# Optimization experiments

Hardware: AMD Instinct MI355X
Metric: run time of the kernel (lower is better)

Reference implementation:

```python
import jax, jax.numpy as jnp
import numpy as np

ALPHA = 0.25
GAMMA = 2.0
# all cost weights are 1.0 per init defaults

def box_cxcywh_to_xyxy(b):
    cx, cy, w, h = b[..., 0], b[..., 1], b[..., 2], b[..., 3]
    return jnp.stack([cx - 0.5 * w, cy - 0.5 * h, cx + 0.5 * w, cy + 0.5 * h], axis=-1)

def generalized_box_iou(b1, b2):
    # b1: [B,Q,4], b2: [B,T,4] in xyxy -> [B,Q,T]
    area1 = (b1[..., 2] - b1[..., 0]) * (b1[..., 3] - b1[..., 1])  # [B,Q]
    area2 = (b2[..., 2] - b2[..., 0]) * (b2[..., 3] - b2[..., 1])  # [B,T]
    lt = jnp.maximum(b1[:, :, None, :2], b2[:, None, :, :2])        # [B,Q,T,2]
    rb = jnp.minimum(b1[:, :, None, 2:], b2[:, None, :, 2:])
    wh = jnp.clip(rb - lt, 0.0)
    inter = wh[..., 0] * wh[..., 1]
    union = area1[:, :, None] + area2[:, None, :] - inter
    iou = inter / union
    lt_c = jnp.minimum(b1[:, :, None, :2], b2[:, None, :, :2])
    rb_c = jnp.maximum(b1[:, :, None, 2:], b2[:, None, :, 2:])
    wh_c = jnp.clip(rb_c - lt_c, 0.0)
    area_c = wh_c[..., 0] * wh_c[..., 1]
    return iou - (area_c - union) / area_c

def point_sample_bilinear(img, pts):
    # img: [B,N,H,W]; pts: [P,2] (x,y) in [0,1]. Matches F.grid_sample
    # bilinear, align_corners=False, padding_mode='zeros'.
    H, W = img.shape[-2], img.shape[-1]
    x = pts[:, 0] * W - 0.5
    y = pts[:, 1] * H - 0.5
    x0 = jnp.floor(x); y0 = jnp.floor(y)
    wx1 = x - x0; wx0 = 1.0 - wx1
    wy1 = y - y0; wy0 = 1.0 - wy1

    def gather(yi, xi):
        valid = ((xi >= 0) & (xi < W) & (yi >= 0) & (yi < H)).astype(img.dtype)
        xc = jnp.clip(xi, 0, W - 1).astype(jnp.int32)
        yc = jnp.clip(yi, 0, H - 1).astype(jnp.int32)
        return img[:, :, yc, xc] * valid  # [B,N,P]

    return (gather(y0, x0) * (wy0 * wx0)
            + gather(y0, x0 + 1) * (wy0 * wx1)
            + gather(y0 + 1, x0) * (wy1 * wx0)
            + gather(y0 + 1, x0 + 1) * (wy1 * wx1))

def point_sample_nearest(img, pts):
    # grid_sample nearest, align_corners=False, zeros padding
    H, W = img.shape[-2], img.shape[-1]
    x = jnp.round(pts[:, 0] * W - 0.5)
    y = jnp.round(pts[:, 1] * H - 0.5)
    valid = ((x >= 0) & (x < W) & (y >= 0) & (y < H)).astype(img.dtype)
    xc = jnp.clip(x, 0, W - 1).astype(jnp.int32)
    yc = jnp.clip(y, 0, H - 1).astype(jnp.int32)
    return img[:, :, yc, xc] * valid  # [B,N,P]

def setup_inputs() -> dict:
    key = jax.random.key(0)
    ks = jax.random.split(key, 7)
    B, Q, C, T, H, W = 2, 900, 91, 64, 128, 128
    P = H * W // 16  # mask_point_sample_ratio = 16
    return {
        "pred_logits": jax.random.normal(ks[0], (B, Q, C), jnp.float32),
        "pred_boxes": jax.random.uniform(ks[1], (B, Q, 4), jnp.float32),
        "pred_masks": jax.random.normal(ks[2], (B, Q, H, W), jnp.float32),
        "tgt_boxes": jax.random.uniform(ks[3], (B, T, 4), jnp.float32),
        "tgt_masks": jax.random.uniform(ks[4], (B, T, H, W), jnp.float32),
        "point_coords": jax.random.uniform(ks[5], (1, P, 2), jnp.float32),
        "tgt_labels": jax.random.randint(ks[6], (B, T), 0, C, jnp.int32),
    }

def reference(pred_logits, pred_boxes, pred_masks, tgt_boxes, tgt_masks, point_coords, tgt_labels):
    # ---- focal classification cost ----
    prob = jax.nn.sigmoid(pred_logits)                          # [B,Q,C]
    neg_cost = (1 - ALPHA) * prob ** GAMMA * (-jax.nn.log_sigmoid(-pred_logits))
    pos_cost = ALPHA * (1 - prob) ** GAMMA * (-jax.nn.log_sigmoid(pred_logits))
    diff = pos_cost - neg_cost                                   # [B,Q,C]
    cost_class = jnp.take_along_axis(diff, tgt_labels[:, None, :], axis=2)  # [B,Q,T]

    # ---- L1 bbox cost (cdist p=1) ----
    cost_bbox = jnp.abs(pred_boxes[:, :, None, :] - tgt_boxes[:, None, :, :]).sum(-1)

    # ---- GIoU cost ----
    giou = generalized_box_iou(box_cxcywh_to_xyxy(pred_boxes), box_cxcywh_to_xyxy(tgt_boxes))

    # ---- point-sampled mask CE / Dice costs ----
    pts = point_coords[0]                                        # [P,2]
    P = pts.shape[0]
    pred_pts = point_sample_bilinear(pred_masks, pts)            # [B,Q,P]
    tgt_pts = point_sample_nearest(tgt_masks, pts)               # [B,T,P]
    pos_ce = -jax.nn.log_sigmoid(pred_pts)
    neg_ce = -jax.nn.log_sigmoid(-pred_pts)
    cost_ce = (jnp.einsum('bqp,btp->bqt', pos_ce, tgt_pts)
               + jnp.einsum('bqp,btp->bqt', neg_ce, 1.0 - tgt_pts)) / P
    s = jax.nn.sigmoid(pred_pts)
    numer = 2.0 * jnp.einsum('bqp,btp->bqt', s, tgt_pts)
    denom = s.sum(-1)[:, :, None] + tgt_pts.sum(-1)[:, None, :]
    cost_dice = 1.0 - (numer + 1.0) / (denom + 1.0)

    C = (cost_bbox + cost_class - giou + cost_ce + cost_dice).astype(jnp.float32)
    # replace non-finite entries by 2 * (per-batch max finite cost)
    fin = jnp.isfinite(C)
    max_cost = jnp.max(jnp.where(fin, C, 0.0), axis=(1, 2), keepdims=True)
    C = jnp.where(fin, C, 2.0 * max_cost)
    return C
```

## Files before the change

### kernel.cpp

```cpp
#include <hip/hip_runtime.h>
#include <hip/hip_bf16.h>
#include <math.h>

#define B_    2
#define Q_    900
#define QPAD_ 912
#define MT_   57
#define CC_   91
#define T_    64
#define H_    128
#define W_    128
#define HW_   (H_*W_)
#define P_    1024
#define NIMG_ (B_*T_ + B_*Q_)
#define IPB_  8
#define FLT_BIG 3.402823466e+38f

#define AS1 __attribute__((address_space(1)))
#define AS3 __attribute__((address_space(3)))

typedef short short8 __attribute__((ext_vector_type(8)));
typedef float f32x4  __attribute__((ext_vector_type(4)));

static __device__ __forceinline__ unsigned short f2bf(float v) {
    __hip_bfloat16 h = __float2bfloat16(v);
    return *reinterpret_cast<unsigned short*>(&h);
}

__global__ __launch_bounds__(256) void kS_sample(
    const float* __restrict__ tgt_masks,
    const float* __restrict__ pred_masks,
    const float* __restrict__ pc,
    unsigned short* __restrict__ tgtPT,
    float* __restrict__ tsumP,
    unsigned short* __restrict__ xsbuf,
    float* __restrict__ lnegP,
    float* __restrict__ lsumP,
    float* __restrict__ bmax)
{
    __shared__ float bufA[HW_];
    __shared__ float bufB[HW_];

    const int tid = threadIdx.x;
    const int wv = tid >> 6, lane = tid & 63;
    const int img0 = blockIdx.x * IPB_;
    const bool isTgt = (img0 < B_*T_);

    if (blockIdx.x == 0 && tid < B_) bmax[tid] = 0.f;

    int   nidx[4];
    int   o[4][4]; float ww[4][4];
    if (isTgt) {
        #pragma unroll
        for (int k = 0; k < 4; ++k) {
            int p = tid*4 + k;
            float px = pc[2*p], py = pc[2*p+1];
            float xf = rintf(px * (float)W_ - 0.5f);
            float yf = rintf(py * (float)H_ - 0.5f);
            bool nv = (xf >= 0.f) && (xf < (float)W_) && (yf >= 0.f) && (yf < (float)H_);
            int xc = (int)fminf(fmaxf(xf, 0.f), (float)(W_-1));
            int yc = (int)fminf(fmaxf(yf, 0.f), (float)(H_-1));
            nidx[k] = nv ? (yc*W_ + xc) : -1;
        }
    } else {
        #pragma unroll
        for (int k = 0; k < 4; ++k) {
            int p = tid*4 + k;
            float px = pc[2*p], py = pc[2*p+1];
            float x = px * (float)W_ - 0.5f;
            float y = py * (float)H_ - 0.5f;
            float x0f = floorf(x), y0f = floorf(y);
            float wx1 = x - x0f, wy1 = y - y0f;
            float wx0 = 1.f - wx1, wy0 = 1.f - wy1;
            int x0 = (int)x0f, y0 = (int)y0f;
            int   xs2[2] = {x0, x0+1}, ys2[2] = {y0, y0+1};
            float wxs[2] = {wx0, wx1}, wys[2] = {wy0, wy1};
            #pragma unroll
            for (int dy = 0; dy < 2; ++dy)
            #pragma unroll
            for (int dx = 0; dx < 2; ++dx) {
                int xi = xs2[dx], yi = ys2[dy];
                bool v = (xi >= 0) && (xi < W_) && (yi >= 0) && (yi < H_);
                int xcc = min(max(xi, 0), W_-1);
                int ycc = min(max(yi, 0), H_-1);
                o [k][dy*2+dx] = ycc*W_ + xcc;
                ww[k][dy*2+dx] = v ? wys[dy]*wxs[dx] : 0.f;
            }
        }
    }

    auto STAGE = [&](int im, float* buf) {
        const float* g = ((im < B_*T_) ? (tgt_masks  + (size_t)im * HW_)
                                       : (pred_masks + (size_t)(im - B_*T_) * HW_))
                         + wv*4096 + lane*4;
        float* l = buf + wv*4096;
        #pragma unroll
        for (int it = 0; it < 16; ++it)
            __builtin_amdgcn_global_load_lds((const AS1 float*)(g + it*256),
                                             (AS3 float*)(l + it*256), 16, 0, 0);
    };

    auto SAMPLE = [&](int im, const float* S) {
        if (isTgt) {
            float vals[4];
            #pragma unroll
            for (int k = 0; k < 4; ++k)
                vals[k] = (nidx[k] >= 0) ? S[nidx[k]] : 0.f;
            *(ushort4*)(tgtPT + (size_t)im*P_ + tid*4) =
                make_ushort4(f2bf(vals[0]), f2bf(vals[1]), f2bf(vals[2]), f2bf(vals[3]));
            float local = (vals[0] + vals[1]) + (vals[2] + vals[3]);
            #pragma unroll
            for (int off = 32; off; off >>= 1) local += __shfl_down(local, off);
            if (lane == 0) tsumP[im*4 + wv] = local;
        } else {
            const int bq = im - B_*T_;
            const int b = bq / Q_, q = bq % Q_;
            float tap[4][4];
            #pragma unroll
            for (int k = 0; k < 4; ++k) {
                tap[k][0] = S[o[k][0]]; tap[k][1] = S[o[k][1]];
                tap[k][2] = S[o[k][2]]; tap[k][3] = S[o[k][3]];
            }
            float ln = 0.f, ls = 0.f;
            unsigned short px_[4], ps_[4];
            #pragma unroll
            for (int k = 0; k < 4; ++k) {
                float x = ww[k][0]*tap[k][0] + ww[k][1]*tap[k][1]
                        + ww[k][2]*tap[k][2] + ww[k][3]*tap[k][3];
                float e  = __expf(-fabsf(x));
                float sp = __logf(1.f + e) + fmaxf(x, 0.f);
                float rr = 1.f / (1.f + e);
                float s  = (x >= 0.f) ? rr : e * rr;
                ln += sp; ls += s;
                px_[k] = f2bf(x); ps_[k] = f2bf(s);
            }
            *(ushort4*)(xsbuf + ((size_t)(b*2+0)*QPAD_ + q)*P_ + tid*4) = make_ushort4(px_[0],px_[1],px_[2],px_[3]);
            *(ushort4*)(xsbuf + ((size_t)(b*2+1)*QPAD_ + q)*P_ + tid*4) = make_ushort4(ps_[0],ps_[1],ps_[2],ps_[3]);
            #pragma unroll
            for (int off = 32; off; off >>= 1) {
                ln += __shfl_down(ln, off);
                ls += __shfl_down(ls, off);
            }
            if (lane == 0) {
                lnegP[(b*Q_ + q)*4 + wv] = ln;
                lsumP[(b*Q_ + q)*4 + wv] = ls;
            }
        }
    };

    STAGE(img0, bufA);
    #pragma unroll
    for (int i = 0; i < IPB_; i += 2) {
        __syncthreads();
        if (i+1 < IPB_) STAGE(img0 + i+1, bufB);
        SAMPLE(img0 + i, bufA);
        __syncthreads();
        if (i+2 < IPB_) STAGE(img0 + i+2, bufA);
        if (i+1 < IPB_) SAMPLE(img0 + i+1, bufB);
    }
}

__global__ __launch_bounds__(256) void k3_gemm(
    const unsigned short* __restrict__ xsbuf,
    const unsigned short* __restrict__ tgtPT,
    const float* __restrict__ lnegP,
    const float* __restrict__ lsumP,
    const float* __restrict__ tsumP,
    const float* __restrict__ pred_logits,
    const float* __restrict__ pred_boxes,
    const float* __restrict__ tgt_boxes,
    const int*   __restrict__ tgt_labels,
    float* __restrict__ out,
    float* __restrict__ bmax)
{
    __shared__ float sT[2][4][4][65];

    const int bid = blockIdx.x;
    const int b = bid / (MT_*4);
    const int rem = bid % (MT_*4);
    const int mt = rem >> 2, nt = rem & 3;
    const int w = threadIdx.x >> 6, l = threadIdx.x & 63;
    const int ml = l & 15, kg = l >> 4;

    const short* Ax = (const short*)xsbuf + ((size_t)(b*2+0)*QPAD_ + mt*16 + ml)*P_ + kg*8 + w*256;
    const short* As = (const short*)xsbuf + ((size_t)(b*2+1)*QPAD_ + mt*16 + ml)*P_ + kg*8 + w*256;
    const short* Bb = (const short*)tgtPT + ((size_t)(b*T_) + nt*16 + ml)*P_ + kg*8 + w*256;

    f32x4 accX = {0,0,0,0};
    f32x4 accS = {0,0,0,0};

    #pragma unroll
    for (int kt = 0; kt < 8; ++kt) {
        const int ko = kt * 32;
        short8 afx = *(const short8*)(Ax + ko);
        short8 afs = *(const short8*)(As + ko);
        short8 bf  = *(const short8*)(Bb + ko);
        accX = __builtin_amdgcn_mfma_f32_16x16x32_bf16(afx, bf, accX, 0, 0, 0);
        accS = __builtin_amdgcn_mfma_f32_16x16x32_bf16(afs, bf, accS, 0, 0, 0);
    }

    #pragma unroll
    for (int r = 0; r < 4; ++r) {
        sT[0][r][w][l] = accX[r];
        sT[1][r][w][l] = accS[r];
    }
    __syncthreads();

    const int tid = threadIdx.x;
    const int ql = tid >> 4, tc = tid & 15;
    const int r   = ql & 3;
    const int src = (ql >> 2)*16 + tc;

    float aX = ((sT[0][r][0][src] + sT[0][r][1][src]) + (sT[0][r][2][src] + sT[0][r][3][src]));
    float aS = ((sT[1][r][0][src] + sT[1][r][1][src]) + (sT[1][r][2][src] + sT[1][r][3][src]));

    const int q = mt*16 + ql;
    const int t = nt*16 + tc;
    const int qc = min(q, Q_-1);

    const float4 tp = *(const float4*)(tsumP + 4*(b*T_ + t));
    const float tsu = (tp.x + tp.y) + (tp.z + tp.w);
    const int   lab = tgt_labels[b*T_ + t];
    const float4 tbx = *(const float4*)(tgt_boxes + (size_t)(b*T_ + t)*4);
    const float4 lp = *(const float4*)(lnegP + 4*(b*Q_ + qc));
    const float4 sp4 = *(const float4*)(lsumP + 4*(b*Q_ + qc));
    float ln  = (lp.x + lp.y) + (lp.z + lp.w);
    float lsv = (sp4.x + sp4.y) + (sp4.z + sp4.w);
    float4 pb = *(const float4*)(pred_boxes + (size_t)(b*Q_ + qc)*4);
    float lg  = pred_logits[((size_t)(b*Q_ + qc))*CC_ + lab];

    float ce   = (ln - aX) * (1.f/(float)P_);
    float dice = 1.f - (2.f*aS + 1.f) / (lsv + tsu + 1.f);

    float e  = __expf(-fabsf(lg));
    float lp2 = log1pf(e);
    float sp_neg = lp2 + fmaxf(-lg, 0.f);
    float sp_pos = lp2 + fmaxf( lg, 0.f);
    float prob = 1.f / (1.f + __expf(-lg));
    float cclass = 0.25f*(1.f-prob)*(1.f-prob)*sp_neg - 0.75f*prob*prob*sp_pos;

    float cbbox = fabsf(pb.x-tbx.x) + fabsf(pb.y-tbx.y) + fabsf(pb.z-tbx.z) + fabsf(pb.w-tbx.w);
    float px1 = pb.x - 0.5f*pb.z, py1 = pb.y - 0.5f*pb.w;
    float px2 = pb.x + 0.5f*pb.z, py2 = pb.y + 0.5f*pb.w;
    float tx1 = tbx.x - 0.5f*tbx.z, ty1 = tbx.y - 0.5f*tbx.w;
    float tx2 = tbx.x + 0.5f*tbx.z, ty2 = tbx.y + 0.5f*tbx.w;
    float a1 = (px2-px1)*(py2-py1);
    float a2 = (tx2-tx1)*(ty2-ty1);
    float iw = fmaxf(fminf(px2,tx2) - fmaxf(px1,tx1), 0.f);
    float ih = fmaxf(fminf(py2,ty2) - fmaxf(py1,ty1), 0.f);
    float inter = iw*ih;
    float uni = a1 + a2 - inter;
    float iou = inter / uni;
    float cw = fmaxf(fmaxf(px2,tx2) - fminf(px1,tx1), 0.f);
    float ch = fmaxf(fmaxf(py2,ty2) - fminf(py1,ty1), 0.f);
    float ac = cw*ch;
    float giou = iou - (ac - uni)/ac;

    float cost = cbbox + cclass - giou + ce + dice;
    float mloc = 0.f;
    if (q < Q_) {
        out[((size_t)(b*Q_ + q))*T_ + t] = cost;
        mloc = (fabsf(cost) <= FLT_BIG) ? fmaxf(cost, 0.f) : 0.f;
    }

    #pragma unroll
    for (int off = 32; off; off >>= 1) mloc = fmaxf(mloc, __shfl_down(mloc, off));
    __shared__ float sm[4];
    if (l == 0) sm[w] = mloc;
    __syncthreads();
    if (tid == 0) {
        float bm = fmaxf(fmaxf(sm[0], sm[1]), fmaxf(sm[2], sm[3]));
        atomicMax((unsigned int*)&bmax[b], __float_as_uint(bm));
    }
}

__global__ __launch_bounds__(256) void k5_fix(float* __restrict__ out,
                                              const float* __restrict__ bmax)
{
    int i = blockIdx.x*256 + threadIdx.x;
    if (i >= B_*Q_*T_) return;
    float v = out[i];
    if (!(fabsf(v) <= FLT_BIG))
        out[i] = 2.f * bmax[i / (Q_*T_)];
}

extern "C" void kernel_launch(void* const* d_in, const int* in_sizes, int n_in,
                              void* d_out, int out_size, void* d_ws, size_t ws_size,
                              hipStream_t stream) {
    const float* pred_logits  = (const float*)d_in[0];
    const float* pred_boxes   = (const float*)d_in[1];
    const float* pred_masks   = (const float*)d_in[2];
    const float* tgt_boxes    = (const float*)d_in[3];
    const float* tgt_masks    = (const float*)d_in[4];
    const float* point_coords = (const float*)d_in[5];
    const int*   tgt_labels   = (const int*)d_in[6];
    float* out = (float*)d_out;

    char* w = (char*)d_ws;
    unsigned short* tgtPT = (unsigned short*)w;
    unsigned short* xsbuf = (unsigned short*)(w + 262144);
    size_t xs_bytes = (size_t)B_*2*QPAD_*P_*2;
    char* w2 = w + 262144 + xs_bytes;
    float* tsumP = (float*)w2;
    float* lnegP = (float*)(w2 + 2048);
    float* lsumP = (float*)(w2 + 2048 + 28800);
    float* bmax  = (float*)(w2 + 2048 + 2*28800);

    kS_sample<<<NIMG_/IPB_, 256, 0, stream>>>(tgt_masks, pred_masks, point_coords,
                                              tgtPT, tsumP, xsbuf, lnegP, lsumP, bmax);
    k3_gemm<<<B_*MT_*4, 256, 0, stream>>>(xsbuf, tgtPT, lnegP, lsumP, tsumP,
                                          pred_logits, pred_boxes, tgt_boxes, tgt_labels, out, bmax);
    k5_fix<<<(B_*Q_*T_ + 255)/256, 256, 0, stream>>>(out, bmax);
}
```

Measured before the change: 40.79 us.

## Sample one mask image per 512-thread block instead of pipelining eight per block

The sampling kernel now launches one block per mask image (2056 blocks of 512 threads) instead of 257 blocks that each double-buffer eight images through LDS. Each block stages a single 64KB image into shared memory and each thread samples two points, so the per-wave partial sums double to eight per image and the GEMM kernel reads them as two float4s. The aim is more parallelism and higher occupancy across CUs in place of the in-block software pipeline. In exchange it gives up load/compute overlap within a block and pays for more block launches and more partial-sum traffic.

```diff
diff --git a/kernel.cpp b/kernel.cpp
--- a/kernel.cpp
+++ b/kernel.cpp
@@ -13,7 +13,6 @@
 #define HW_   (H_*W_)
 #define P_    1024
 #define NIMG_ (B_*T_ + B_*Q_)
-#define IPB_  8
 #define FLT_BIG 3.402823466e+38f
 
 #define AS1 __attribute__((address_space(1)))
@@ -27,7 +26,7 @@
     return *reinterpret_cast<unsigned short*>(&h);
 }
 
-__global__ __launch_bounds__(256) void kS_sample(
+__global__ __launch_bounds__(512) void kS_sample(
     const float* __restrict__ tgt_masks,
     const float* __restrict__ pred_masks,
     const float* __restrict__ pc,
@@ -38,22 +37,32 @@
     float* __restrict__ lsumP,
     float* __restrict__ bmax)
 {
-    __shared__ float bufA[HW_];
-    __shared__ float bufB[HW_];
+    __shared__ float simg[HW_];
 
     const int tid = threadIdx.x;
     const int wv = tid >> 6, lane = tid & 63;
-    const int img0 = blockIdx.x * IPB_;
-    const bool isTgt = (img0 < B_*T_);
+    const bool isTgt = (blockIdx.x < (B_*T_));
+    const float* __restrict__ img = isTgt
+        ? (tgt_masks  + (size_t)blockIdx.x * HW_)
+        : (pred_masks + (size_t)(blockIdx.x - B_*T_) * HW_);
+
+    {
+        const float* g = img  + wv*2048 + lane*4;
+        float*       l = simg + wv*2048;
+        #pragma unroll
+        for (int it = 0; it < 8; ++it)
+            __builtin_amdgcn_global_load_lds((const AS1 float*)(g + it*256),
+                                             (AS3 float*)(l + it*256), 16, 0, 0);
+    }
 
     if (blockIdx.x == 0 && tid < B_) bmax[tid] = 0.f;
 
-    int   nidx[4];
-    int   o[4][4]; float ww[4][4];
     if (isTgt) {
-        #pragma unroll
-        for (int k = 0; k < 4; ++k) {
-            int p = tid*4 + k;
+        const int bt = blockIdx.x;
+        int nidx[2];
+        #pragma unroll
+        for (int k = 0; k < 2; ++k) {
+            int p = tid*2 + k;
             float px = pc[2*p], py = pc[2*p+1];
             float xf = rintf(px * (float)W_ - 0.5f);
             float yf = rintf(py * (float)H_ - 0.5f);
@@ -62,10 +71,25 @@
             int yc = (int)fminf(fmaxf(yf, 0.f), (float)(H_-1));
             nidx[k] = nv ? (yc*W_ + xc) : -1;
         }
+        __syncthreads();
+
+        float v0 = (nidx[0] >= 0) ? simg[nidx[0]] : 0.f;
+        float v1 = (nidx[1] >= 0) ? simg[nidx[1]] : 0.f;
+        *(ushort2*)(tgtPT + (size_t)bt*P_ + tid*2) = make_ushort2(f2bf(v0), f2bf(v1));
+
+        float local = v0 + v1;
+        #pragma unroll
+        for (int off = 32; off; off >>= 1) local += __shfl_down(local, off);
+        if (lane == 0) tsumP[bt*8 + wv] = local;
     } else {
-        #pragma unroll
-        for (int k = 0; k < 4; ++k) {
-            int p = tid*4 + k;
+        const int bq = blockIdx.x - B_*T_;
+        const int b = bq / Q_, q = bq % Q_;
+
+        int   o[2][4];
+        float ww[2][4];
+        #pragma unroll
+        for (int k = 0; k < 2; ++k) {
+            int p = tid*2 + k;
             float px = pc[2*p], py = pc[2*p+1];
             float x = px * (float)W_ - 0.5f;
             float y = py * (float)H_ - 0.5f;
@@ -87,76 +111,41 @@
                 ww[k][dy*2+dx] = v ? wys[dy]*wxs[dx] : 0.f;
             }
         }
-    }
-
-    auto STAGE = [&](int im, float* buf) {
-        const float* g = ((im < B_*T_) ? (tgt_masks  + (size_t)im * HW_)
-                                       : (pred_masks + (size_t)(im - B_*T_) * HW_))
-                         + wv*4096 + lane*4;
-        float* l = buf + wv*4096;
-        #pragma unroll
-        for (int it = 0; it < 16; ++it)
-            __builtin_amdgcn_global_load_lds((const AS1 float*)(g + it*256),
-                                             (AS3 float*)(l + it*256), 16, 0, 0);
-    };
-
-    auto SAMPLE = [&](int im, const float* S) {
-        if (isTgt) {
-            float vals[4];
-            #pragma unroll
-            for (int k = 0; k < 4; ++k)
-                vals[k] = (nidx[k] >= 0) ? S[nidx[k]] : 0.f;
-            *(ushort4*)(tgtPT + (size_t)im*P_ + tid*4) =
-                make_ushort4(f2bf(vals[0]), f2bf(vals[1]), f2bf(vals[2]), f2bf(vals[3]));
-            float local = (vals[0] + vals[1]) + (vals[2] + vals[3]);
-            #pragma unroll
-            for (int off = 32; off; off >>= 1) local += __shfl_down(local, off);
-            if (lane == 0) tsumP[im*4 + wv] = local;
-        } else {
-            const int bq = im - B_*T_;
-            const int b = bq / Q_, q = bq % Q_;
-            float tap[4][4];
-            #pragma unroll
-            for (int k = 0; k < 4; ++k) {
-                tap[k][0] = S[o[k][0]]; tap[k][1] = S[o[k][1]];
-                tap[k][2] = S[o[k][2]]; tap[k][3] = S[o[k][3]];
-            }
-            float ln = 0.f, ls = 0.f;
-            unsigned short px_[4], ps_[4];
-            #pragma unroll
-            for (int k = 0; k < 4; ++k) {
-                float x = ww[k][0]*tap[k][0] + ww[k][1]*tap[k][1]
-                        + ww[k][2]*tap[k][2] + ww[k][3]*tap[k][3];
-                float e  = __expf(-fabsf(x));
-                float sp = __logf(1.f + e) + fmaxf(x, 0.f);
-                float rr = 1.f / (1.f + e);
-                float s  = (x >= 0.f) ? rr : e * rr;
-                ln += sp; ls += s;
-                px_[k] = f2bf(x); ps_[k] = f2bf(s);
-            }
-            *(ushort4*)(xsbuf + ((size_t)(b*2+0)*QPAD_ + q)*P_ + tid*4) = make_ushort4(px_[0],px_[1],px_[2],px_[3]);
-            *(ushort4*)(xsbuf + ((size_t)(b*2+1)*QPAD_ + q)*P_ + tid*4) = make_ushort4(ps_[0],ps_[1],ps_[2],ps_[3]);
-            #pragma unroll
-            for (int off = 32; off; off >>= 1) {
-                ln += __shfl_down(ln, off);
-                ls += __shfl_down(ls, off);
-            }
-            if (lane == 0) {
-                lnegP[(b*Q_ + q)*4 + wv] = ln;
-                lsumP[(b*Q_ + q)*4 + wv] = ls;
-            }
-        }
-    };
-
-    STAGE(img0, bufA);
-    #pragma unroll
-    for (int i = 0; i < IPB_; i += 2) {
         __syncthreads();
-        if (i+1 < IPB_) STAGE(img0 + i+1, bufB);
-        SAMPLE(img0 + i, bufA);
-        __syncthreads();
-        if (i+2 < IPB_) STAGE(img0 + i+2, bufA);
-        if (i+1 < IPB_) SAMPLE(img0 + i+1, bufB);
+
+        float tap[2][4];
+        #pragma unroll
+        for (int k = 0; k < 2; ++k) {
+            tap[k][0] = simg[o[k][0]]; tap[k][1] = simg[o[k][1]];
+            tap[k][2] = simg[o[k][2]]; tap[k][3] = simg[o[k][3]];
+        }
+
+        float ln = 0.f, ls = 0.f;
+        unsigned short px_[2], ps_[2];
+        #pragma unroll
+        for (int k = 0; k < 2; ++k) {
+            float x = ww[k][0]*tap[k][0] + ww[k][1]*tap[k][1]
+                    + ww[k][2]*tap[k][2] + ww[k][3]*tap[k][3];
+            float e  = __expf(-fabsf(x));
+            float sp = __logf(1.f + e) + fmaxf(x, 0.f);
+            float rr = 1.f / (1.f + e);
+            float s  = (x >= 0.f) ? rr : e * rr;
+            ln += sp; ls += s;
+            px_[k] = f2bf(x); ps_[k] = f2bf(s);
+        }
+
+        *(ushort2*)(xsbuf + ((size_t)(b*2+0)*QPAD_ + q)*P_ + tid*2) = make_ushort2(px_[0], px_[1]);
+        *(ushort2*)(xsbuf + ((size_t)(b*2+1)*QPAD_ + q)*P_ + tid*2) = make_ushort2(ps_[0], ps_[1]);
+
+        #pragma unroll
+        for (int off = 32; off; off >>= 1) {
+            ln += __shfl_down(ln, off);
+            ls += __shfl_down(ls, off);
+        }
+        if (lane == 0) {
+            lnegP[(b*Q_ + q)*8 + wv] = ln;
+            lsumP[(b*Q_ + q)*8 + wv] = ls;
+        }
     }
 }
 
@@ -218,14 +207,17 @@
     const int t = nt*16 + tc;
     const int qc = min(q, Q_-1);
 
-    const float4 tp = *(const float4*)(tsumP + 4*(b*T_ + t));
-    const float tsu = (tp.x + tp.y) + (tp.z + tp.w);
+    const float4* tpp = (const float4*)(tsumP + 8*(b*T_ + t));
+    float4 tp0 = tpp[0], tp1 = tpp[1];
+    const float tsu = ((tp0.x+tp0.y)+(tp0.z+tp0.w)) + ((tp1.x+tp1.y)+(tp1.z+tp1.w));
     const int   lab = tgt_labels[b*T_ + t];
     const float4 tbx = *(const float4*)(tgt_boxes + (size_t)(b*T_ + t)*4);
-    const float4 lp = *(const float4*)(lnegP + 4*(b*Q_ + qc));
-    const float4 sp4 = *(const float4*)(lsumP + 4*(b*Q_ + qc));
-    float ln  = (lp.x + lp.y) + (lp.z + lp.w);
-    float lsv = (sp4.x + sp4.y) + (sp4.z + sp4.w);
+    const float4* lpp = (const float4*)(lnegP + 8*(b*Q_ + qc));
+    float4 lp0 = lpp[0], lp1 = lpp[1];
+    float ln  = ((lp0.x+lp0.y)+(lp0.z+lp0.w)) + ((lp1.x+lp1.y)+(lp1.z+lp1.w));
+    const float4* spp = (const float4*)(lsumP + 8*(b*Q_ + qc));
+    float4 sp0 = spp[0], sp1 = spp[1];
+    float lsv = ((sp0.x+sp0.y)+(sp0.z+sp0.w)) + ((sp1.x+sp1.y)+(sp1.z+sp1.w));
     float4 pb = *(const float4*)(pred_boxes + (size_t)(b*Q_ + qc)*4);
     float lg  = pred_logits[((size_t)(b*Q_ + qc))*CC_ + lab];
 
@@ -302,12 +294,12 @@
     size_t xs_bytes = (size_t)B_*2*QPAD_*P_*2;
     char* w2 = w + 262144 + xs_bytes;
     float* tsumP = (float*)w2;
-    float* lnegP = (float*)(w2 + 2048);
-    float* lsumP = (float*)(w2 + 2048 + 28800);
-    float* bmax  = (float*)(w2 + 2048 + 2*28800);
-
-    kS_sample<<<NIMG_/IPB_, 256, 0, stream>>>(tgt_masks, pred_masks, point_coords,
-                                              tgtPT, tsumP, xsbuf, lnegP, lsumP, bmax);
+    float* lnegP = (float*)(w2 + 4096);
+    float* lsumP = (float*)(w2 + 4096 + 57600);
+    float* bmax  = (float*)(w2 + 4096 + 2*57600);
+
+    kS_sample<<<NIMG_, 512, 0, stream>>>(tgt_masks, pred_masks, point_coords,
+                                         tgtPT, tsumP, xsbuf, lnegP, lsumP, bmax);
     k3_gemm<<<B_*MT_*4, 256, 0, stream>>>(xsbuf, tgtPT, lnegP, lsumP, tsumP,
                                           pred_logits, pred_boxes, tgt_boxes, tgt_labels, out, bmax);
     k5_fix<<<(B_*Q_*T_ + 255)/256, 256, 0, stream>>>(out, bmax);
```

After: 39.54 us. 3.1% less time.
